# Optimization experiments

Hardware: AMD Instinct MI355X
Metric: run time of the kernel (lower is better)

## Reference

```python
import jax, jax.numpy as jnp
import numpy as np

ALPHA = 1.702
LIMIT = 7.0


def setup_inputs() -> dict:
    key = jax.random.key(0)
    ks = jax.random.split(key, 7)
    B, S, H, D, E, TOPK = 2, 2048, 2048, 2048, 8, 4
    T = B * S
    hidden_states = jax.random.normal(ks[0], (B, S, H), dtype=jnp.float32)
    gate_up_proj = jax.random.normal(ks[1], (E, H, 2 * D), dtype=jnp.float32) * 0.02
    gate_up_proj_bias = jax.random.normal(ks[2], (E, 2 * D), dtype=jnp.float32) * 0.02
    down_proj = jax.random.normal(ks[3], (E, D, H), dtype=jnp.float32) * 0.02
    down_proj_bias = jax.random.normal(ks[4], (E, H), dtype=jnp.float32) * 0.02
    rw = jax.random.uniform(ks[5], (T, E), dtype=jnp.float32)
    routing_weights = rw / jnp.sum(rw, axis=-1, keepdims=True)
    router_indices = jax.random.randint(ks[6], (T, TOPK), 0, E, dtype=jnp.int64)
    return {
        "hidden_states": hidden_states,
        "gate_up_proj": gate_up_proj,
        "gate_up_proj_bias": gate_up_proj_bias,
        "down_proj": down_proj,
        "down_proj_bias": down_proj_bias,
        "routing_weights": routing_weights,
        "router_indices": router_indices,
    }


def geglu(gate_up):
    # interleaved layout: gate = [..., 0::2], up = [..., 1::2]
    gate = gate_up[..., 0::2]
    up = gate_up[..., 1::2]
    gate = jnp.minimum(gate, LIMIT)
    up = jnp.clip(up, -LIMIT, LIMIT)
    glu = gate * jax.nn.sigmoid(gate * ALPHA)
    return (up + 1.0) * glu


def reference(hidden_states, gate_up_proj, gate_up_proj_bias, down_proj,
              down_proj_bias, routing_weights, router_indices):
    B, S, H = hidden_states.shape
    x = hidden_states.reshape(-1, H)  # [T, H]
    # per-expert batched GEMM: [E, T, 2D]
    gate_up = jnp.einsum('th,ehd->etd', x, gate_up_proj) + gate_up_proj_bias[:, None, :]
    act = geglu(gate_up)  # [E, T, D]
    out = jnp.einsum('etd,edh->eth', act, down_proj) + down_proj_bias[:, None, :]
    # weight by router probs and sum over experts
    out = out * routing_weights.T[:, :, None]  # [E, T, H]
    out = jnp.sum(out, axis=0)
    return out.reshape(B, S, H)
```

## Files before the change

### kernel.cpp

```cpp
#include <hip/hip_runtime.h>
#include <hip/hip_bf16.h>

#define ALPHA 1.702f
#define GLIMIT 7.0f

typedef __attribute__((ext_vector_type(4))) float f32x4;
typedef __attribute__((ext_vector_type(8))) __bf16 bf16x8;
typedef __attribute__((ext_vector_type(8))) short short8;

typedef __attribute__((address_space(3))) unsigned int as3_uint;
typedef const __attribute__((address_space(1))) unsigned int as1_uint;

__device__ __forceinline__ void async_copy16(void* lds, const void* g) {
    __builtin_amdgcn_global_load_lds((as1_uint*)g, (as3_uint*)lds, 16, 0, 0);
}

__device__ __forceinline__ short f2bf(float f) {
    unsigned u = __float_as_uint(f);
    unsigned r = (u + 0x7fffu + ((u >> 16) & 1u)) >> 16;
    return (short)r;
}

__global__ void cvt_bf16_kernel(const float* __restrict__ src,
                                short* __restrict__ dst, int n4) {
    int i = blockIdx.x * blockDim.x + threadIdx.x;
    if (i < n4) {
        float4 v = reinterpret_cast<const float4*>(src)[i];
        short4 o;
        o.x = f2bf(v.x); o.y = f2bf(v.y); o.z = f2bf(v.z); o.w = f2bf(v.w);
        reinterpret_cast<short4*>(dst)[i] = o;
    }
}

__global__ void transpose_cvt(const float* __restrict__ src,
                              short* __restrict__ dst, int R, int C, int perm) {
    __shared__ float t[64][65];
    const int z  = blockIdx.z;
    const int c0 = blockIdx.x * 64;
    const int r0 = blockIdx.y * 64;
    const float* s = src + (size_t)z * R * C;
    short* d = dst + (size_t)z * R * C;
    const int tid = threadIdx.x;
#pragma unroll
    for (int i = 0; i < 16; ++i) {
        int idx = i * 256 + tid;
        int r = idx >> 6, c = idx & 63;
        t[r][c] = s[(size_t)(r0 + r) * C + c0 + c];
    }
    __syncthreads();
#pragma unroll
    for (int i = 0; i < 16; ++i) {
        int idx = i * 256 + tid;
        int r = idx >> 6, c = idx & 63;
        int rr = c0 + r;
        int rloc = rr & 255;
        int rp = perm ? ((rr & ~255) | ((rloc & 1) << 7) | (rloc >> 1)) : rr;
        d[(size_t)rp * R + r0 + c] = f2bf(t[c][r]);
    }
}


struct Gemm1PSrc {
    const short* A; const short* B;
    __device__ __forceinline__ const short* operator()(int t, int h) const {
        int e = t >> 5;
        size_t ko = (size_t)(t & 31) << 6;
        if (h & 2) return B + ((size_t)e << 23) + ((size_t)(h & 1) << 18) + ko;
        return A + ((size_t)(h & 1) << 18) + ko;
    }
};

struct Gemm2Src {
    const short* act; const short* wdt; size_t aoff, boff; int kh;
    __device__ __forceinline__ const short* operator()(int t, int h) const {
        int g = (kh << 7) + t;
        int e = g >> 5;
        size_t ko = (size_t)(g & 31) << 6;
        if (h & 2) return wdt + ((size_t)e << 22) + boff + ((size_t)(h & 1) << 18) + ko;
        return act + ((size_t)e << 23) + aoff + ((size_t)(h & 1) << 18) + ko;
    }
};

#define PH_BAR()  __builtin_amdgcn_s_barrier()
#define PH_LGKM() do { asm volatile("s_waitcnt lgkmcnt(0)" ::: "memory"); \
                       __builtin_amdgcn_sched_barrier(0); } while (0)
#define VMW(n)    asm volatile("s_waitcnt vmcnt(" #n ")" ::: "memory")

template <int NT, int SEG, typename Src, typename Epi>
__device__ __forceinline__ void gemm_8phase(const Src& src, char* smem,
                                            f32x4 (&acc)[8][4], const Epi& epi) {
    const int tid  = threadIdx.x;
    const int lane = tid & 63;
    const int wid  = tid >> 6;
    const int wr   = wid >> 2;
    const int wcol = wid & 3;
    const int lhi  = lane >> 4;
    const int llo  = lane & 15;

    auto stage = [&](int buf, int h, const short* g) {
        char* dst = smem + buf * 65536 + h * 16384;
        {
            int c = tid, r = c >> 3, s = (c & 7) ^ (r & 7);
            async_copy16(dst + c * 16, g + (size_t)r * 2048 + s * 8);
        }
        {
            int c = tid + 512, r = c >> 3, s = (c & 7) ^ (r & 7);
            async_copy16(dst + c * 16, g + (size_t)r * 2048 + s * 8);
        }
    };
    auto ldfrag = [&](int buf, int h, int row, int slot) {
        return *(const bf16x8*)(smem + buf * 65536 + h * 16384 + row * 128 +
                                ((slot ^ (row & 7)) << 4));
    };

    stage(0, 0, src(0, 0)); stage(0, 2, src(0, 2));
    stage(0, 3, src(0, 3)); stage(0, 1, src(0, 1));
    stage(1, 0, src(1, 0)); stage(1, 2, src(1, 2)); stage(1, 3, src(1, 3));
    VMW(8);
    PH_BAR();

    bf16x8 a[4][2], b[4][2];
#pragma unroll
    for (int n = 0; n < 2; ++n) {
        int row = wcol * 32 + n * 16 + llo;
        b[n][0] = ldfrag(0, 2, row, lhi);
        b[n][1] = ldfrag(0, 2, row, 4 + lhi);
    }

    for (int t = 0; t < NT; ++t) {
        const int cur = t & 1, nxt = cur ^ 1;
#pragma unroll
        for (int m = 0; m < 4; ++m) {
            int row = wr * 64 + m * 16 + llo;
            a[m][0] = ldfrag(cur, 0, row, lhi);
            a[m][1] = ldfrag(cur, 0, row, 4 + lhi);
        }
        if (t + 1 < NT) stage(nxt, 1, src(t + 1, 1));
        PH_BAR(); PH_LGKM();
        __builtin_amdgcn_s_setprio(1);
#pragma unroll
        for (int m = 0; m < 4; ++m)
#pragma unroll
            for (int n = 0; n < 2; ++n)
#pragma unroll
                for (int ks = 0; ks < 2; ++ks)
                    acc[m][n] = __builtin_amdgcn_mfma_f32_16x16x32_bf16(
                        a[m][ks], b[n][ks], acc[m][n], 0, 0, 0);
        __builtin_amdgcn_s_setprio(0);
        PH_BAR();
#pragma unroll
        for (int n = 0; n < 2; ++n) {
            int row = wcol * 32 + n * 16 + llo;
            b[2 + n][0] = ldfrag(cur, 3, row, lhi);
            b[2 + n][1] = ldfrag(cur, 3, row, 4 + lhi);
        }
        if (t + 2 < NT) { stage(cur, 0, src(t + 2, 0)); VMW(10); }
        else if (t + 1 < NT) { VMW(8); }
        else { VMW(0); }
        PH_BAR(); PH_LGKM();
        __builtin_amdgcn_s_setprio(1);
#pragma unroll
        for (int m = 0; m < 4; ++m)
#pragma unroll
            for (int n = 2; n < 4; ++n)
#pragma unroll
                for (int ks = 0; ks < 2; ++ks)
                    acc[m][n] = __builtin_amdgcn_mfma_f32_16x16x32_bf16(
                        a[m][ks], b[n][ks], acc[m][n], 0, 0, 0);
        __builtin_amdgcn_s_setprio(0);
        PH_BAR();
#pragma unroll
        for (int m = 0; m < 4; ++m) {
            int row = wr * 64 + m * 16 + llo;
            a[m][0] = ldfrag(cur, 1, row, lhi);
            a[m][1] = ldfrag(cur, 1, row, 4 + lhi);
        }
        if (t + 2 < NT) stage(cur, 2, src(t + 2, 2));
        PH_BAR(); PH_LGKM();
        __builtin_amdgcn_s_setprio(1);
#pragma unroll
        for (int m = 0; m < 4; ++m)
#pragma unroll
            for (int n = 0; n < 2; ++n)
#pragma unroll
                for (int ks = 0; ks < 2; ++ks)
                    acc[4 + m][n] = __builtin_amdgcn_mfma_f32_16x16x32_bf16(
                        a[m][ks], b[n][ks], acc[4 + m][n], 0, 0, 0);
        __builtin_amdgcn_s_setprio(0);
        PH_BAR();
        if (t + 2 < NT) { stage(cur, 3, src(t + 2, 3)); VMW(8); }
        else if (t + 1 < NT) { VMW(2); }
        else { VMW(0); }
        PH_BAR(); PH_LGKM();
        __builtin_amdgcn_s_setprio(1);
        if (t + 1 < NT) {
#pragma unroll
            for (int n = 0; n < 2; ++n) {
                int row = wcol * 32 + n * 16 + llo;
                b[n][0] = ldfrag(nxt, 2, row, lhi);
                b[n][1] = ldfrag(nxt, 2, row, 4 + lhi);
            }
        }
#pragma unroll
        for (int m = 0; m < 4; ++m)
#pragma unroll
            for (int n = 2; n < 4; ++n)
#pragma unroll
                for (int ks = 0; ks < 2; ++ks)
                    acc[4 + m][n] = __builtin_amdgcn_mfma_f32_16x16x32_bf16(
                        a[m][ks], b[n][ks], acc[4 + m][n], 0, 0, 0);
        __builtin_amdgcn_s_setprio(0);
        PH_BAR();
        if (((t + 1) & (SEG - 1)) == 0) {
            epi(t / SEG, acc);
            if (t + 1 < NT) {
#pragma unroll
                for (int m = 0; m < 8; ++m)
#pragma unroll
                    for (int n = 0; n < 4; ++n)
                        acc[m][n] = (f32x4){0.f, 0.f, 0.f, 0.f};
            }
        }
    }
}

__global__ __launch_bounds__(512, 2) void gemm1_8ph(
    const short* __restrict__ xb, const short* __restrict__ wgut,
    const float* __restrict__ bias, const float* __restrict__ rwp,
    short* __restrict__ act) {
    __shared__ __align__(16) char smem[131072];
    __shared__ float rws2[2048];
    __shared__ float bias2[2048];
    const int bid = blockIdx.x;
    const int xcd = bid & 7, j = bid >> 3;
    const int m0 = (((xcd << 1) + (j >> 4)) << 8);
    const int n0 = ((j & 15) << 8);
    const int tid  = threadIdx.x;
    const int lane = tid & 63;
    const int wid  = tid >> 6;
    const int wr = wid >> 2, wcol = wid & 3;
    const int lhi = lane >> 4, llo = lane & 15;

    ((float4*)rws2)[tid] = ((const float4*)(rwp + (size_t)m0 * 8))[tid];
    {
        int idx = tid << 2;
        int ei = idx >> 8, c = idx & 255;
        ((float4*)bias2)[tid] =
            *(const float4*)(bias + (size_t)ei * 4096 + n0 + c);
    }

    f32x4 acc[8][4];
#pragma unroll
    for (int m = 0; m < 8; ++m)
#pragma unroll
        for (int n = 0; n < 4; ++n) acc[m][n] = (f32x4){0.f, 0.f, 0.f, 0.f};

    Gemm1PSrc src{ xb + (size_t)m0 * 2048, wgut + (size_t)n0 * 2048 };
    const int a0 = n0 >> 1;

    auto epi = [&](int e, f32x4 (&ac)[8][4]) {
        short* acte = act + ((size_t)e << 23);
        float bg[2], bu[2];
#pragma unroll
        for (int n = 0; n < 2; ++n) {
            int acol = wcol * 32 + n * 16 + llo;
            bg[n] = bias2[(e << 8) + 2 * acol];
            bu[n] = bias2[(e << 8) + 2 * acol + 1];
        }
        PH_LGKM();
        PH_BAR();
#pragma unroll
        for (int c = 0; c < 4; ++c) {
            char* slot = smem + ((c & 1) ? 32768 : 81920);
#pragma unroll
            for (int mb = 0; mb < 2; ++mb) {
                int m = 2 * c + mb;
                int rowb = (m >> 2) * 128 + wr * 64 + (m & 3) * 16 + (lhi << 2);
#pragma unroll
                for (int n = 0; n < 2; ++n) {
                    int acol = wcol * 32 + n * 16 + llo;
#pragma unroll
                    for (int q = 0; q < 4; ++q) {
                        float g = ac[m][n][q] + bg[n];
                        float u = ac[m][n + 2][q] + bu[n];
                        g = fminf(g, GLIMIT);
                        u = fmaxf(fminf(u, GLIMIT), -GLIMIT);
                        float glu = g / (1.f + __expf(-ALPHA * g));
                        float aa = (u + 1.f) * glu * rws2[(rowb + q) * 8 + e];
                        int lrow = wr * 32 + mb * 16 + (lhi << 2) + q;
                        *(short*)(slot + lrow * 256 +
                                  (((acol << 1) ^ ((lrow & 15) << 4)))) = f2bf(aa);
                    }
                }
            }
            PH_LGKM();
            PH_BAR();
#pragma unroll
            for (int i = 0; i < 2; ++i) {
                int idx = i * 512 + tid;
                int lrow = idx >> 4, g16 = idx & 15;
                int grow = ((c >> 1) << 7) + ((lrow >> 5) << 6) +
                           (((c & 1) * 2 + ((lrow >> 4) & 1)) << 4) + (lrow & 15);
                short8 vv = *(const short8*)(slot + lrow * 256 +
                                             ((g16 ^ (lrow & 15)) << 4));
                *(short8*)(acte + (size_t)(m0 + grow) * 2048 + a0 + g16 * 8) = vv;
            }
        }
        PH_BAR();
    };
    gemm_8phase<256, 32>(src, smem, acc, epi);
}

__global__ __launch_bounds__(512, 2) void gemm2_8ph(
    const short* __restrict__ act, const short* __restrict__ wdt,
    float* __restrict__ out, float* __restrict__ part) {
    __shared__ __align__(16) char smem[131072];
    const int kh = blockIdx.z;
    int flat = blockIdx.x + (blockIdx.y << 3);
    int swz = (flat & 7) * 16 + (flat >> 3);
    const int n0 = (swz & 7) * 256;
    const int m0 = (swz >> 3) * 256;
    const int tid  = threadIdx.x;
    const int lane = tid & 63;
    const int wid  = tid >> 6;
    const int wr = wid >> 2, wcol = wid & 3;

    f32x4 acc[8][4];
#pragma unroll
    for (int m = 0; m < 8; ++m)
#pragma unroll
        for (int n = 0; n < 4; ++n) acc[m][n] = (f32x4){0.f, 0.f, 0.f, 0.f};

    Gemm2Src src{ act, wdt, (size_t)m0 * 2048, (size_t)n0 * 2048, kh };
    float* dst = (kh == 0) ? out : part;

    auto epi = [&](int, f32x4 (&ac)[8][4]) {
#pragma unroll
        for (int m = 0; m < 8; ++m) {
            int row = m0 + (m >> 2) * 128 + wr * 64 + (m & 3) * 16 + ((lane >> 4) << 2);
#pragma unroll
            for (int n = 0; n < 4; ++n) {
                int col = n0 + (n >> 1) * 128 + wcol * 32 + (n & 1) * 16 + (lane & 15);
#pragma unroll
                for (int q = 0; q < 4; ++q)
                    dst[(size_t)(row + q) * 2048 + col] = ac[m][n][q];
            }
        }
    };
    gemm_8phase<128, 128>(src, smem, acc, epi);
}

__global__ __launch_bounds__(256) void reduce_bias(
    const float* __restrict__ p1, const float* __restrict__ rw,
    const float* __restrict__ bd, float* __restrict__ out) {
    const int t = blockIdx.x;
    const int tid = threadIdx.x;
    float rwv[8];
#pragma unroll
    for (int e = 0; e < 8; ++e) rwv[e] = rw[(size_t)t * 8 + e];
    size_t base = (size_t)t * 2048;
#pragma unroll
    for (int i = 0; i < 2; ++i) {
        int h = (tid + i * 256) * 4;
        f32x4 o = *(const f32x4*)(out + base + h);
        f32x4 p = *(const f32x4*)(p1 + base + h);
        o += p;
#pragma unroll
        for (int e = 0; e < 8; ++e) {
            f32x4 bb = *(const f32x4*)(bd + e * 2048 + h);
            o += rwv[e] * bb;
        }
        *(f32x4*)(out + base + h) = o;
    }
}

extern "C" void kernel_launch(void* const* d_in, const int* in_sizes, int n_in,
                              void* d_out, int out_size, void* d_ws, size_t ws_size,
                              hipStream_t stream) {
    const float* x   = (const float*)d_in[0];
    const float* wgu = (const float*)d_in[1];
    const float* bgu = (const float*)d_in[2];
    const float* wd  = (const float*)d_in[3];
    const float* bd  = (const float*)d_in[4];
    const float* rw  = (const float*)d_in[5];
    float* out = (float*)d_out;

    char* ws = (char*)d_ws;
    short* xb   = (short*)(ws);
    short* wgut = (short*)(ws + 16777216);
    float* p1   = (float*)(ws + 16777216);
    short* wdt  = (short*)(ws + 150994944);
    short* actb = (short*)(ws + 218103808);

    cvt_bf16_kernel<<<8192, 256, 0, stream>>>(x, xb, 2097152);
    transpose_cvt<<<dim3(64, 32, 8), 256, 0, stream>>>(wgu, wgut, 2048, 4096, 1);
    transpose_cvt<<<dim3(32, 32, 8), 256, 0, stream>>>(wd, wdt, 2048, 2048, 0);
    gemm1_8ph<<<256, 512, 0, stream>>>(xb, wgut, bgu, rw, actb);
    gemm2_8ph<<<dim3(8, 16, 2), 512, 0, stream>>>(actb, wdt, out, p1);
    reduce_bias<<<4096, 256, 0, stream>>>(p1, rw, bd, out);
}
```

Baseline: 938.2 us.

## Swap GEMM1 operand roles so epilogue writes activations directly without LDS staging

GEMM1 now treats the permuted gate/up weights as the A operand and tokens as B. The accumulator layout then places consecutive D columns in each lane's registers, so the GEGLU epilogue can pack four bf16 values and store them straight to global memory. This drops the LDS round trip and the extra barriers the old epilogue needed. In exchange the global stores are 8-byte short4 writes instead of 16-byte coalesced ones, and the expert index wraps with &7.

New measurement: 896.3 us. 4.5% less time.

```diff
diff --git a/kernel.cpp b/kernel.cpp
--- a/kernel.cpp
+++ b/kernel.cpp
@@ -60,13 +60,13 @@
 }
 
 
-struct Gemm1PSrc {
+struct Gemm1TSrc {
     const short* A; const short* B;
     __device__ __forceinline__ const short* operator()(int t, int h) const {
-        int e = t >> 5;
+        int e = (t >> 5) & 7;
         size_t ko = (size_t)(t & 31) << 6;
-        if (h & 2) return B + ((size_t)e << 23) + ((size_t)(h & 1) << 18) + ko;
-        return A + ((size_t)(h & 1) << 18) + ko;
+        if (h & 2) return B + ((size_t)(h & 1) << 18) + ko;
+        return A + ((size_t)e << 23) + ((size_t)(h & 1) << 18) + ko;
     }
 };
 
@@ -224,8 +224,8 @@
     }
 }
 
-__global__ __launch_bounds__(512, 2) void gemm1_8ph(
-    const short* __restrict__ xb, const short* __restrict__ wgut,
+__global__ __launch_bounds__(512, 2) void gemm1_main(
+    const short* __restrict__ xb, const short* __restrict__ wgutp,
     const float* __restrict__ bias, const float* __restrict__ rwp,
     short* __restrict__ act) {
     __shared__ __align__(16) char smem[131072];
@@ -233,20 +233,20 @@
     __shared__ float bias2[2048];
     const int bid = blockIdx.x;
     const int xcd = bid & 7, j = bid >> 3;
-    const int m0 = (((xcd << 1) + (j >> 4)) << 8);
-    const int n0 = ((j & 15) << 8);
+    const int t0 = (((xcd << 1) + (j >> 4)) << 8);
+    const int p0 = ((j & 15) << 8);
     const int tid  = threadIdx.x;
     const int lane = tid & 63;
     const int wid  = tid >> 6;
     const int wr = wid >> 2, wcol = wid & 3;
     const int lhi = lane >> 4, llo = lane & 15;
 
-    ((float4*)rws2)[tid] = ((const float4*)(rwp + (size_t)m0 * 8))[tid];
+    ((float4*)rws2)[tid] = ((const float4*)(rwp + (size_t)t0 * 8))[tid];
     {
         int idx = tid << 2;
         int ei = idx >> 8, c = idx & 255;
         ((float4*)bias2)[tid] =
-            *(const float4*)(bias + (size_t)ei * 4096 + n0 + c);
+            *(const float4*)(bias + (size_t)ei * 4096 + p0 + c);
     }
 
     f32x4 acc[8][4];
@@ -255,58 +255,39 @@
 #pragma unroll
         for (int n = 0; n < 4; ++n) acc[m][n] = (f32x4){0.f, 0.f, 0.f, 0.f};
 
-    Gemm1PSrc src{ xb + (size_t)m0 * 2048, wgut + (size_t)n0 * 2048 };
-    const int a0 = n0 >> 1;
-
-    auto epi = [&](int e, f32x4 (&ac)[8][4]) {
+    Gemm1TSrc src{ wgutp + (size_t)p0 * 2048, xb + (size_t)t0 * 2048 };
+    const int dbase = (p0 >> 1) + wr * 64;
+
+    auto epi = [&](int s, f32x4 (&ac)[8][4]) {
+        int e = s & 7;
         short* acte = act + ((size_t)e << 23);
-        float bg[2], bu[2];
-#pragma unroll
-        for (int n = 0; n < 2; ++n) {
-            int acol = wcol * 32 + n * 16 + llo;
-            bg[n] = bias2[(e << 8) + 2 * acol];
-            bu[n] = bias2[(e << 8) + 2 * acol + 1];
-        }
-        PH_LGKM();
-        PH_BAR();
-#pragma unroll
-        for (int c = 0; c < 4; ++c) {
-            char* slot = smem + ((c & 1) ? 32768 : 81920);
-#pragma unroll
-            for (int mb = 0; mb < 2; ++mb) {
-                int m = 2 * c + mb;
-                int rowb = (m >> 2) * 128 + wr * 64 + (m & 3) * 16 + (lhi << 2);
-#pragma unroll
-                for (int n = 0; n < 2; ++n) {
-                    int acol = wcol * 32 + n * 16 + llo;
-#pragma unroll
-                    for (int q = 0; q < 4; ++q) {
-                        float g = ac[m][n][q] + bg[n];
-                        float u = ac[m][n + 2][q] + bu[n];
-                        g = fminf(g, GLIMIT);
-                        u = fmaxf(fminf(u, GLIMIT), -GLIMIT);
-                        float glu = g / (1.f + __expf(-ALPHA * g));
-                        float aa = (u + 1.f) * glu * rws2[(rowb + q) * 8 + e];
-                        int lrow = wr * 32 + mb * 16 + (lhi << 2) + q;
-                        *(short*)(slot + lrow * 256 +
-                                  (((acol << 1) ^ ((lrow & 15) << 4)))) = f2bf(aa);
-                    }
+#pragma unroll
+        for (int m = 0; m < 4; ++m) {
+            float bg[4], bu[4];
+#pragma unroll
+            for (int q = 0; q < 4; ++q) {
+                int jj = wr * 64 + m * 16 + (lhi << 2) + q;
+                bg[q] = bias2[(e << 8) + 2 * jj];
+                bu[q] = bias2[(e << 8) + 2 * jj + 1];
+            }
+            int dc0 = dbase + m * 16 + (lhi << 2);
+#pragma unroll
+            for (int n = 0; n < 4; ++n) {
+                int tloc = ((n >> 1) << 7) + wcol * 32 + ((n & 1) << 4) + llo;
+                float w = rws2[tloc * 8 + e];
+                short4 o;
+#pragma unroll
+                for (int q = 0; q < 4; ++q) {
+                    float g = ac[m][n][q] + bg[q];
+                    float u = ac[4 + m][n][q] + bu[q];
+                    g = fminf(g, GLIMIT);
+                    u = fmaxf(fminf(u, GLIMIT), -GLIMIT);
+                    float glu = g / (1.f + __expf(-ALPHA * g));
+                    ((short*)&o)[q] = f2bf((u + 1.f) * glu * w);
                 }
-            }
-            PH_LGKM();
-            PH_BAR();
-#pragma unroll
-            for (int i = 0; i < 2; ++i) {
-                int idx = i * 512 + tid;
-                int lrow = idx >> 4, g16 = idx & 15;
-                int grow = ((c >> 1) << 7) + ((lrow >> 5) << 6) +
-                           (((c & 1) * 2 + ((lrow >> 4) & 1)) << 4) + (lrow & 15);
-                short8 vv = *(const short8*)(slot + lrow * 256 +
-                                             ((g16 ^ (lrow & 15)) << 4));
-                *(short8*)(acte + (size_t)(m0 + grow) * 2048 + a0 + g16 * 8) = vv;
-            }
-        }
-        PH_BAR();
+                *(short4*)(acte + (size_t)(t0 + tloc) * 2048 + dc0) = o;
+            }
+        }
     };
     gemm_8phase<256, 32>(src, smem, acc, epi);
 }
@@ -395,7 +376,7 @@
     cvt_bf16_kernel<<<8192, 256, 0, stream>>>(x, xb, 2097152);
     transpose_cvt<<<dim3(64, 32, 8), 256, 0, stream>>>(wgu, wgut, 2048, 4096, 1);
     transpose_cvt<<<dim3(32, 32, 8), 256, 0, stream>>>(wd, wdt, 2048, 2048, 0);
-    gemm1_8ph<<<256, 512, 0, stream>>>(xb, wgut, bgu, rw, actb);
+    gemm1_main<<<256, 512, 0, stream>>>(xb, wgut, bgu, rw, actb);
     gemm2_8ph<<<dim3(8, 16, 2), 512, 0, stream>>>(actb, wdt, out, p1);
     reduce_bias<<<4096, 256, 0, stream>>>(p1, rw, bd, out);
 }
```
